# Kernel optimization log

Measured on AMD Instinct MI355X. Metric: run time of the kernel, lower is better.

Reference implementation:

```python
import jax, jax.numpy as jnp
import numpy as np
from jax import lax

NL, C, NH, LV, NPT, DFF = 6, 256, 8, 4, 4, 1024
DH = C // NH
SHAPES = np.array([[100, 100], [50, 50], [25, 25], [13, 13]], dtype=np.int32)
STARTS = np.concatenate([[0], np.cumsum(SHAPES[:, 0] * SHAPES[:, 1])[:-1]]).astype(np.int32)
S_TOT = int((SHAPES[:, 0] * SHAPES[:, 1]).sum())
TOPK = 30


def _ln(x, g, b, eps=1e-5):
    m = x.mean(-1, keepdims=True)
    v = ((x - m) ** 2).mean(-1, keepdims=True)
    return (x - m) * lax.rsqrt(v + eps) * g + b


def _mha(q, k, v, Wqkv, bqkv, Wo, bo):
    # torch nn.MultiheadAttention math (batch-first view), dropout=eval
    N, Q, _ = q.shape
    def proj(x, W, b):
        return (x @ W.T + b).reshape(N, -1, NH, DH)
    qh = proj(q, Wqkv[:C], bqkv[:C]) * (DH ** -0.5)
    kh = proj(k, Wqkv[C:2 * C], bqkv[C:2 * C])
    vh = proj(v, Wqkv[2 * C:], bqkv[2 * C:])
    a = jax.nn.softmax(jnp.einsum('bqhd,bkhd->bhqk', qh, kh), axis=-1)
    o = jnp.einsum('bhqk,bkhd->bqhd', a, vh).reshape(N, Q, C)
    return o @ Wo + bo


def _bilinear(img, gx, gy):
    # img [B,H,W,D]; gx,gy [B,P] pixel coords; grid_sample align_corners=False, zero pad
    B, Hh, Ww, D = img.shape
    x0 = jnp.floor(gx)
    y0 = jnp.floor(gy)
    wx = gx - x0
    wy = gy - y0
    bidx = jnp.arange(B)[:, None]
    def tap(xi, yi):
        inb = (xi >= 0) & (xi < Ww) & (yi >= 0) & (yi < Hh)
        v = img[bidx, jnp.clip(yi, 0, Hh - 1).astype(jnp.int32), jnp.clip(xi, 0, Ww - 1).astype(jnp.int32)]
        return v * inb[..., None]
    return (tap(x0, y0) * ((1 - wx) * (1 - wy))[..., None]
            + tap(x0 + 1, y0) * (wx * (1 - wy))[..., None]
            + tap(x0, y0 + 1) * ((1 - wx) * wy)[..., None]
            + tap(x0 + 1, y0 + 1) * (wx * wy)[..., None])


def _msda(q, ref, src, Wv, bv, Woff, boff, Waw, baw, Wo, bo):
    # MSDeformAttn: value proj, per-query sampling offsets + softmax weights,
    # multi-level bilinear sampling, weighted sum, output proj.
    N, Q, _ = q.shape
    value = (src @ Wv + bv).reshape(N, S_TOT, NH, DH)
    off = (q @ Woff + boff).reshape(N, Q, NH, LV, NPT, 2)
    aw = jax.nn.softmax((q @ Waw + baw).reshape(N, Q, NH, LV * NPT), -1).reshape(N, Q, NH, LV, NPT)
    norm = jnp.asarray(SHAPES[:, ::-1], jnp.float32)  # (W_l, H_l)
    loc = ref[:, :, None, :, None, :] + off / norm[None, None, None, :, None, :]
    acc = jnp.zeros((N * NH, Q, DH), src.dtype)
    for l in range(LV):
        H_, W_ = int(SHAPES[l, 0]), int(SHAPES[l, 1])
        s = int(STARTS[l])
        v_l = value[:, s:s + H_ * W_].transpose(0, 2, 1, 3).reshape(N * NH, H_, W_, DH)
        gx = loc[:, :, :, l, :, 0].transpose(0, 2, 1, 3).reshape(N * NH, Q * NPT) * W_ - 0.5
        gy = loc[:, :, :, l, :, 1].transpose(0, 2, 1, 3).reshape(N * NH, Q * NPT) * H_ - 0.5
        samp = _bilinear(v_l, gx, gy).reshape(N * NH, Q, NPT, DH)
        w_l = aw[:, :, :, l].transpose(0, 2, 1, 3).reshape(N * NH, Q, NPT)
        acc = acc + (samp * w_l[..., None]).sum(2)
    out = acc.reshape(N, NH, Q, DH).transpose(0, 2, 1, 3).reshape(N, Q, C)
    return out @ Wo + bo, loc, aw


def _decoder(tgt, reference_points, src, valid_ratios, query_pos, P):
    ref_in = reference_points[:, :, None] * valid_ratios[:, None]  # [N,Q,LV,2]
    out = tgt
    for i in range(NL):
        q = out + query_pos
        sa = _mha(q, q, out, P['Wqkv'][i], P['bqkv'][i], P['Wmo'][i], P['bmo'][i])
        out = _ln(out + sa, P['ln2g'][i], P['ln2b'][i])
        ca, loc, aw = _msda(out + query_pos, ref_in, src, P['Wv'][i], P['bv'][i], P['Woff'][i],
                            P['boff'][i], P['Waw'][i], P['baw'][i], P['Wo'][i], P['bo'][i])
        out = _ln(out + ca, P['ln1g'][i], P['ln1b'][i])
        ffn = jax.nn.relu(out @ P['W1'][i] + P['b1'][i]) @ P['W2'][i] + P['b2'][i]
        out = _ln(out + ffn, P['ln3g'][i], P['ln3b'][i])
        loc = loc / valid_ratios[:, None, None, :, None, :]
    N, Q = loc.shape[:2]
    wflat = aw.reshape(N, Q, -1)           # [N,Q,NH*LV*NPT]
    sflat = loc.reshape(N, Q, -1, 2)
    _, top_idx = lax.top_k(wflat, TOPK)
    samples_keep = jnp.take_along_axis(sflat, top_idx[..., None], axis=2)
    return out, reference_points, samples_keep


def setup_inputs() -> dict:
    key = jax.random.key(0)
    ks = iter(jax.random.split(key, 64))
    N, Q = 4, 300
    d = {}
    d['tgt'] = jax.random.normal(next(ks), (N, Q, C), jnp.float32)
    d['reference_points'] = jax.random.uniform(next(ks), (N, Q, 2), jnp.float32)
    d['src'] = jax.random.normal(next(ks), (N, S_TOT, C), jnp.float32)
    d['src_spatial_shapes'] = jnp.asarray(SHAPES, jnp.int32)
    d['src_level_start_index'] = jnp.asarray(STARTS, jnp.int32)
    d['src_valid_ratios'] = jnp.ones((N, LV, 2), jnp.float32)
    d['query_pos'] = jax.random.normal(next(ks), (N, Q, C), jnp.float32) * 0.02
    def p(shape, scale=0.02):
        return jax.random.normal(next(ks), shape, jnp.float32) * scale
    d['Wv'] = p((NL, C, C)); d['bv'] = jnp.zeros((NL, C))
    d['Woff'] = p((NL, C, NH * LV * NPT * 2)); d['boff'] = p((NL, NH * LV * NPT * 2), 0.1)
    d['Waw'] = p((NL, C, NH * LV * NPT)); d['baw'] = jnp.zeros((NL, NH * LV * NPT))
    d['Wo'] = p((NL, C, C)); d['bo'] = jnp.zeros((NL, C))
    d['Wqkv'] = p((NL, 3 * C, C)); d['bqkv'] = jnp.zeros((NL, 3 * C))
    d['Wmo'] = p((NL, C, C)); d['bmo'] = jnp.zeros((NL, C))
    for n in ('ln1', 'ln2', 'ln3'):
        d[n + 'g'] = jnp.ones((NL, C)); d[n + 'b'] = jnp.zeros((NL, C))
    d['W1'] = p((NL, C, DFF)); d['b1'] = jnp.zeros((NL, DFF))
    d['W2'] = p((NL, DFF, C)); d['b2'] = jnp.zeros((NL, C))
    return d


def reference(tgt, reference_points, src, src_spatial_shapes, src_level_start_index,
              src_valid_ratios, query_pos, Wv, bv, Woff, boff, Waw, baw, Wo, bo,
              Wqkv, bqkv, Wmo, bmo, ln1g, ln1b, ln2g, ln2b, ln3g, ln3b, W1, b1, W2, b2):
    # src_spatial_shapes / src_level_start_index are static (SHAPES/STARTS)
    P = dict(Wv=Wv, bv=bv, Woff=Woff, boff=boff, Waw=Waw, baw=baw, Wo=Wo, bo=bo,
             Wqkv=Wqkv, bqkv=bqkv, Wmo=Wmo, bmo=bmo, ln1g=ln1g, ln1b=ln1b,
             ln2g=ln2g, ln2b=ln2b, ln3g=ln3g, ln3b=ln3b, W1=W1, b1=b1, W2=W2, b2=b2)
    return _decoder(tgt, reference_points, src, src_valid_ratios, query_pos, P)
```

## Files before the change

### kernel.cpp

```cpp
#include <hip/hip_runtime.h>
#include <hip/hip_bf16.h>
#include <math.h>

constexpr int kNL = 6, kC = 256, kNH = 8, kDH = 32, kLV = 4, kNPT = 4;
constexpr int kDFF = 1024, kNB = 4, kNQ = 300, kSTOT = 13294, kTOPK = 30;
constexpr int kNTOK = kNB * kNQ;
constexpr int kMV = kNB * kSTOT;

constexpr size_t kWST      = 950272;
constexpr size_t OFF_QKV   = 0;
constexpr size_t OFF_MO    = 196608;
constexpr size_t OFF_OFFAW = 262144;
constexpr size_t OFF_O     = 360448;
constexpr size_t OFF_W1    = 425984;
constexpr size_t OFF_W2    = 688128;

constexpr size_t A_KH = 0;
constexpr size_t A_KL = 311296;
constexpr size_t A_VH = 622592;
constexpr size_t A_VL = 950272;
constexpr size_t A_TOT = 1277952;

typedef __bf16 bf16x8 __attribute__((ext_vector_type(8)));
typedef float f32x4 __attribute__((ext_vector_type(4)));

__device__ __forceinline__ unsigned short f2bf(float f) {
  unsigned int u = __float_as_uint(f);
  unsigned int r = (u + 0x7fffu + ((u >> 16) & 1u)) >> 16;
  return (unsigned short)r;
}
__device__ __forceinline__ void split2(float x, unsigned short& h, unsigned short& l) {
  h = f2bf(x);
  float hf = __uint_as_float(((unsigned int)h) << 16);
  l = f2bf(x - hf);
}
union BF8 { unsigned short u[8]; bf16x8 v; };

constexpr int SB_PREP = 1200;
constexpr int SB_CSRC = 13294;
constexpr int SB_CWV  = 1536;
constexpr int SB_WQ   = 4608;
constexpr int SB_T1   = 384;
constexpr int SB_T2   = 384;
constexpr int SB_T3   = 192;
constexpr int SB_T4   = 384;
constexpr int SB_T5   = 1536;
constexpr int SB_T6   = 1536;
constexpr int SB_VPAD = 80;
constexpr int SB_TOTAL = SB_PREP + SB_CSRC + SB_CWV + SB_WQ + SB_T1 + SB_T2 +
                         SB_T3 + SB_T4 + SB_T5 + SB_T6 + SB_VPAD;

__device__ __forceinline__ void wsplitT_body(
    const float* __restrict__ src, unsigned short* __restrict__ dh,
    unsigned short* __restrict__ dl, int K, int N, size_t dstOff,
    int idx, int nbx, int nby, float t[32][33], int tid) {
  const int bx = idx % nbx;
  const int by = (idx / nbx) % nby;
  const int layer = idx / (nbx * nby);
  const int nb = bx * 32, kb = by * 32;
  const float* s = src + (size_t)layer * K * N;
  unsigned short* ph = dh + (size_t)layer * kWST + dstOff;
  unsigned short* pl = dl + (size_t)layer * kWST + dstOff;
  const int tx = tid & 31, ty = tid >> 5;
  for (int i = ty; i < 32; i += 8)
    t[i][tx] = s[(size_t)(kb + i) * N + nb + tx];
  __syncthreads();
  for (int i = ty; i < 32; i += 8) {
    unsigned short h, l;
    split2(t[tx][i], h, l);
    ph[(size_t)(nb + i) * K + kb + tx] = h;
    pl[(size_t)(nb + i) * K + kb + tx] = l;
  }
}

__global__ __launch_bounds__(256) void setup_kernel(
    const float* __restrict__ tgt, const float* __restrict__ qpos,
    float* __restrict__ out_buf, float* __restrict__ qbuf,
    const float* __restrict__ src, unsigned short* __restrict__ src_bf,
    const float* __restrict__ Wv, unsigned short* __restrict__ wv_bf,
    const float* __restrict__ Wqkv, const float* __restrict__ Wmo,
    const float* __restrict__ Woff, const float* __restrict__ Waw,
    const float* __restrict__ Wo, const float* __restrict__ W1,
    const float* __restrict__ W2,
    unsigned short* __restrict__ whi, unsigned short* __restrict__ wlo,
    unsigned short* __restrict__ KV) {
  __shared__ float t[32][33];
  const int tid = threadIdx.x;
  int b = blockIdx.x;

  if (b < SB_PREP) {
    int i = b * 256 + tid;
    float v = tgt[i];
    out_buf[i] = v;
    qbuf[i] = v + qpos[i];
    return;
  }
  b -= SB_PREP;
  if (b < SB_CSRC) {
    int i = b * 256 + tid;
    float4 v = ((const float4*)src)[i];
    ushort4 o;
    o.x = f2bf(v.x); o.y = f2bf(v.y); o.z = f2bf(v.z); o.w = f2bf(v.w);
    ((ushort4*)src_bf)[i] = o;
    return;
  }
  b -= SB_CSRC;
  if (b < SB_CWV) {
    int l = b >> 8, n = b & 255, k = tid;
    wv_bf[(size_t)b * 256 + k] = f2bf(Wv[((size_t)l * 256 + k) * 256 + n]);
    return;
  }
  b -= SB_CWV;
  if (b < SB_WQ) {
    int layer = b / 768;
    int i = (b % 768) * 256 + tid;
    float v = Wqkv[(size_t)layer * 196608 + i];
    unsigned short h, l;
    split2(v, h, l);
    whi[(size_t)layer * kWST + OFF_QKV + i] = h;
    wlo[(size_t)layer * kWST + OFF_QKV + i] = l;
    return;
  }
  b -= SB_WQ;
  if (b < SB_T1) { wsplitT_body(Wmo,  whi, wlo, 256, 256,  OFF_MO,    b, 8,  8, t, tid); return; }
  b -= SB_T1;
  if (b < SB_T2) { wsplitT_body(Woff, whi, wlo, 256, 256,  OFF_OFFAW, b, 8,  8, t, tid); return; }
  b -= SB_T2;
  if (b < SB_T3) { wsplitT_body(Waw,  whi, wlo, 256, 128,  OFF_OFFAW + 256 * 256, b, 4, 8, t, tid); return; }
  b -= SB_T3;
  if (b < SB_T4) { wsplitT_body(Wo,   whi, wlo, 256, 256,  OFF_O,     b, 8,  8, t, tid); return; }
  b -= SB_T4;
  if (b < SB_T5) { wsplitT_body(W1,   whi, wlo, 256, 1024, OFF_W1,    b, 32, 8, t, tid); return; }
  b -= SB_T5;
  if (b < SB_T6) { wsplitT_body(W2,   whi, wlo, 1024, 256, OFF_W2,    b, 8, 32, t, tid); return; }
  b -= SB_T6;
  {
    int i = b * 256 + tid;
    if (i < 32 * 32 * 20) {
      int j = 300 + i % 20;
      int rest = i / 20;
      size_t idx = (size_t)rest * 320 + j;
      KV[A_VH + idx] = 0;
      KV[A_VL + idx] = 0;
    }
  }
}

template <bool RELU, int CM>
__global__ __launch_bounds__(256) void gemm_pw(
    const float* __restrict__ A,
    const unsigned short* __restrict__ BH, const unsigned short* __restrict__ BL,
    const float* __restrict__ bias, float* __restrict__ C1,
    float* __restrict__ C2,
    int M, int N, int K) {
  constexpr int LDK = 40;
  __shared__ __align__(16) unsigned short Ah[2][64 * LDK], Al[2][64 * LDK];
  __shared__ __align__(16) unsigned short Bh[2][64 * LDK], Bl[2][64 * LDK];
  const int tid = threadIdx.x;
  const int wid = tid >> 6, lane = tid & 63;
  const int wm = wid & 1, wn = wid >> 1;
  const int quad = lane >> 4, l16 = lane & 15;
  const int m0 = blockIdx.y * 64, n0 = blockIdx.x * 64;
  f32x4 acc[2][2] = {};

  const int r = tid >> 2, seg = tid & 3;
  int gr = m0 + r;
  if (gr >= M) gr = M - 1;
  const float* aRow = A + (size_t)gr * K + seg * 8;
  const unsigned short* bhRow = BH + (size_t)(n0 + r) * K + seg * 8;
  const unsigned short* blRow = BL + (size_t)(n0 + r) * K + seg * 8;

  float4 ra0 = *(const float4*)(aRow);
  float4 ra1 = *(const float4*)(aRow + 4);
  uint4 rbh = *(const uint4*)(bhRow);
  uint4 rbl = *(const uint4*)(blRow);

  {
    float xs[8] = {ra0.x, ra0.y, ra0.z, ra0.w, ra1.x, ra1.y, ra1.z, ra1.w};
    unsigned short h[8], l[8];
#pragma unroll
    for (int i = 0; i < 8; ++i) split2(xs[i], h[i], l[i]);
    *(ushort4*)&Ah[0][r * LDK + seg * 8] = make_ushort4(h[0], h[1], h[2], h[3]);
    *(ushort4*)&Ah[0][r * LDK + seg * 8 + 4] = make_ushort4(h[4], h[5], h[6], h[7]);
    *(ushort4*)&Al[0][r * LDK + seg * 8] = make_ushort4(l[0], l[1], l[2], l[3]);
    *(ushort4*)&Al[0][r * LDK + seg * 8 + 4] = make_ushort4(l[4], l[5], l[6], l[7]);
    *(uint4*)&Bh[0][r * LDK + seg * 8] = rbh;
    *(uint4*)&Bl[0][r * LDK + seg * 8] = rbl;
  }
  if (K > 32) {
    ra0 = *(const float4*)(aRow + 32);
    ra1 = *(const float4*)(aRow + 36);
    rbh = *(const uint4*)(bhRow + 32);
    rbl = *(const uint4*)(blRow + 32);
  }
  __syncthreads();

  const int NK = K / 32;
  for (int ks = 0; ks < NK; ++ks) {
    const int cur = ks & 1;
    if (ks + 1 < NK) {
      float xs[8] = {ra0.x, ra0.y, ra0.z, ra0.w, ra1.x, ra1.y, ra1.z, ra1.w};
      unsigned short h[8], l[8];
#pragma unroll
      for (int i = 0; i < 8; ++i) split2(xs[i], h[i], l[i]);
      *(ushort4*)&Ah[cur ^ 1][r * LDK + seg * 8] = make_ushort4(h[0], h[1], h[2], h[3]);
      *(ushort4*)&Ah[cur ^ 1][r * LDK + seg * 8 + 4] = make_ushort4(h[4], h[5], h[6], h[7]);
      *(ushort4*)&Al[cur ^ 1][r * LDK + seg * 8] = make_ushort4(l[0], l[1], l[2], l[3]);
      *(ushort4*)&Al[cur ^ 1][r * LDK + seg * 8 + 4] = make_ushort4(l[4], l[5], l[6], l[7]);
      *(uint4*)&Bh[cur ^ 1][r * LDK + seg * 8] = rbh;
      *(uint4*)&Bl[cur ^ 1][r * LDK + seg * 8] = rbl;
      if (ks + 2 < NK) {
        ra0 = *(const float4*)(aRow + (ks + 2) * 32);
        ra1 = *(const float4*)(aRow + (ks + 2) * 32 + 4);
        rbh = *(const uint4*)(bhRow + (ks + 2) * 32);
        rbl = *(const uint4*)(blRow + (ks + 2) * 32);
      }
    }
    bf16x8 ah[2], al[2], bh[2], bl[2];
#pragma unroll
    for (int mt = 0; mt < 2; ++mt) {
      ah[mt] = *(const bf16x8*)&Ah[cur][(wm * 32 + mt * 16 + l16) * LDK + quad * 8];
      al[mt] = *(const bf16x8*)&Al[cur][(wm * 32 + mt * 16 + l16) * LDK + quad * 8];
    }
#pragma unroll
    for (int nt = 0; nt < 2; ++nt) {
      bh[nt] = *(const bf16x8*)&Bh[cur][(wn * 32 + nt * 16 + l16) * LDK + quad * 8];
      bl[nt] = *(const bf16x8*)&Bl[cur][(wn * 32 + nt * 16 + l16) * LDK + quad * 8];
    }
#pragma unroll
    for (int mt = 0; mt < 2; ++mt)
#pragma unroll
      for (int nt = 0; nt < 2; ++nt) {
        acc[mt][nt] = __builtin_amdgcn_mfma_f32_16x16x32_bf16(ah[mt], bh[nt], acc[mt][nt], 0, 0, 0);
        acc[mt][nt] = __builtin_amdgcn_mfma_f32_16x16x32_bf16(ah[mt], bl[nt], acc[mt][nt], 0, 0, 0);
        acc[mt][nt] = __builtin_amdgcn_mfma_f32_16x16x32_bf16(al[mt], bh[nt], acc[mt][nt], 0, 0, 0);
      }
    __syncthreads();
  }

  float bc[2];
#pragma unroll
  for (int nt = 0; nt < 2; ++nt) {
    int col = n0 + wn * 32 + nt * 16 + l16;
    bc[nt] = (CM == 3 && col >= 256) ? 0.f : bias[col];
  }
#pragma unroll
  for (int mt = 0; mt < 2; ++mt) {
#pragma unroll
    for (int i = 0; i < 4; ++i) {
      int row = m0 + wm * 32 + mt * 16 + quad * 4 + i;
      if (row < M) {
#pragma unroll
        for (int nt = 0; nt < 2; ++nt) {
          int col = n0 + wn * 32 + nt * 16 + l16;
          float val = acc[mt][nt][i] + bc[nt];
          if (RELU) val = fmaxf(val, 0.f);
          if (CM == 3) {
            if (col < 256) C1[(size_t)row * 256 + col] = val;
            else C2[(size_t)row * 128 + col - 256] = val;
          } else {
            C1[(size_t)row * N + col] = val;
          }
        }
      }
    }
  }
}

__global__ __launch_bounds__(256) void qkv_value_kernel(
    const float* __restrict__ A, const float* __restrict__ A2,
    const unsigned short* __restrict__ BH, const unsigned short* __restrict__ BL,
    const float* __restrict__ bias, float* __restrict__ C1,
    unsigned short* __restrict__ C3,
    const unsigned short* __restrict__ Abf, const unsigned short* __restrict__ Btbf,
    const float* __restrict__ biasv, float* __restrict__ Cv) {
  __shared__ union __align__(16) {
    struct { unsigned short Ah[2][64 * 40], Al[2][64 * 40],
                            Bh[2][64 * 40], Bl[2][64 * 40]; } q;
    struct { unsigned short As[2][128 * 32], Bs[2][128 * 32]; } v;
  } sm;
  const int tid = threadIdx.x;
  const int wid = tid >> 6, lane = tid & 63;
  const int quad = lane >> 4, l16 = lane & 15;

  if (blockIdx.x < 228) {
    constexpr int LDK = 40, M = 1200, K = 256;
    const int m0 = (blockIdx.x / 12) * 64, n0 = (blockIdx.x % 12) * 64;
    const int wm = wid & 1, wn = wid >> 1;
    const float* Ause = (n0 >= 512) ? A2 : A;
    f32x4 acc[2][2] = {};

    const int r = tid >> 2, seg = tid & 3;
    int gr = m0 + r;
    if (gr >= M) gr = M - 1;
    const float* aRow = Ause + (size_t)gr * K + seg * 8;
    const unsigned short* bhRow = BH + (size_t)(n0 + r) * K + seg * 8;
    const unsigned short* blRow = BL + (size_t)(n0 + r) * K + seg * 8;

    float4 ra0 = *(const float4*)(aRow);
    float4 ra1 = *(const float4*)(aRow + 4);
    uint4 rbh = *(const uint4*)(bhRow);
    uint4 rbl = *(const uint4*)(blRow);
    {
      float xs[8] = {ra0.x, ra0.y, ra0.z, ra0.w, ra1.x, ra1.y, ra1.z, ra1.w};
      unsigned short h[8], l[8];
#pragma unroll
      for (int i = 0; i < 8; ++i) split2(xs[i], h[i], l[i]);
      *(ushort4*)&sm.q.Ah[0][r * LDK + seg * 8] = make_ushort4(h[0], h[1], h[2], h[3]);
      *(ushort4*)&sm.q.Ah[0][r * LDK + seg * 8 + 4] = make_ushort4(h[4], h[5], h[6], h[7]);
      *(ushort4*)&sm.q.Al[0][r * LDK + seg * 8] = make_ushort4(l[0], l[1], l[2], l[3]);
      *(ushort4*)&sm.q.Al[0][r * LDK + seg * 8 + 4] = make_ushort4(l[4], l[5], l[6], l[7]);
      *(uint4*)&sm.q.Bh[0][r * LDK + seg * 8] = rbh;
      *(uint4*)&sm.q.Bl[0][r * LDK + seg * 8] = rbl;
    }
    ra0 = *(const float4*)(aRow + 32);
    ra1 = *(const float4*)(aRow + 36);
    rbh = *(const uint4*)(bhRow + 32);
    rbl = *(const uint4*)(blRow + 32);
    __syncthreads();

    const int NK = K / 32;
    for (int ks = 0; ks < NK; ++ks) {
      const int cur = ks & 1;
      if (ks + 1 < NK) {
        float xs[8] = {ra0.x, ra0.y, ra0.z, ra0.w, ra1.x, ra1.y, ra1.z, ra1.w};
        unsigned short h[8], l[8];
#pragma unroll
        for (int i = 0; i < 8; ++i) split2(xs[i], h[i], l[i]);
        *(ushort4*)&sm.q.Ah[cur ^ 1][r * LDK + seg * 8] = make_ushort4(h[0], h[1], h[2], h[3]);
        *(ushort4*)&sm.q.Ah[cur ^ 1][r * LDK + seg * 8 + 4] = make_ushort4(h[4], h[5], h[6], h[7]);
        *(ushort4*)&sm.q.Al[cur ^ 1][r * LDK + seg * 8] = make_ushort4(l[0], l[1], l[2], l[3]);
        *(ushort4*)&sm.q.Al[cur ^ 1][r * LDK + seg * 8 + 4] = make_ushort4(l[4], l[5], l[6], l[7]);
        *(uint4*)&sm.q.Bh[cur ^ 1][r * LDK + seg * 8] = rbh;
        *(uint4*)&sm.q.Bl[cur ^ 1][r * LDK + seg * 8] = rbl;
        if (ks + 2 < NK) {
          ra0 = *(const float4*)(aRow + (ks + 2) * 32);
          ra1 = *(const float4*)(aRow + (ks + 2) * 32 + 4);
          rbh = *(const uint4*)(bhRow + (ks + 2) * 32);
          rbl = *(const uint4*)(blRow + (ks + 2) * 32);
        }
      }
      bf16x8 ah[2], al[2], bh[2], bl[2];
#pragma unroll
      for (int mt = 0; mt < 2; ++mt) {
        ah[mt] = *(const bf16x8*)&sm.q.Ah[cur][(wm * 32 + mt * 16 + l16) * LDK + quad * 8];
        al[mt] = *(const bf16x8*)&sm.q.Al[cur][(wm * 32 + mt * 16 + l16) * LDK + quad * 8];
      }
#pragma unroll
// ... 151 lines not shown
  for (int i = 0; i < 8; ++i) split2(qs[i], qh.u[i], ql.u[i]);

  f32x4 S[19];
#pragma unroll
  for (int t = 0; t < 19; ++t) {
    bf16x8 kh = *(const bf16x8*)&kh_g[(t * 16 + l16) * 32 + quad * 8];
    bf16x8 kl = *(const bf16x8*)&kl_g[(t * 16 + l16) * 32 + quad * 8];
    f32x4 z = {0.f, 0.f, 0.f, 0.f};
    z = __builtin_amdgcn_mfma_f32_16x16x32_bf16(qh.v, kh, z, 0, 0, 0);
    z = __builtin_amdgcn_mfma_f32_16x16x32_bf16(qh.v, kl, z, 0, 0, 0);
    z = __builtin_amdgcn_mfma_f32_16x16x32_bf16(ql.v, kh, z, 0, 0, 0);
    S[t] = z;
  }
  float mx[4] = {-1e30f, -1e30f, -1e30f, -1e30f};
#pragma unroll
  for (int t = 0; t < 19; ++t) {
#pragma unroll
    for (int i = 0; i < 4; ++i) {
      float s = S[t][i] * scale;
      if (t == 18 && l16 >= 12) s = -1e30f;
      S[t][i] = s;
      mx[i] = fmaxf(mx[i], s);
    }
  }
#pragma unroll
  for (int i = 0; i < 4; ++i) {
#pragma unroll
    for (int off = 8; off > 0; off >>= 1) mx[i] = fmaxf(mx[i], __shfl_xor(mx[i], off));
  }
  float sm[4] = {0.f, 0.f, 0.f, 0.f};
#pragma unroll
  for (int t = 0; t < 19; ++t) {
#pragma unroll
    for (int i = 0; i < 4; ++i) {
      float e = expf(S[t][i] - mx[i]);
      S[t][i] = e;
      sm[i] += e;
    }
  }
#pragma unroll
  for (int i = 0; i < 4; ++i) {
#pragma unroll
    for (int off = 8; off > 0; off >>= 1) sm[i] += __shfl_xor(sm[i], off);
  }
  f32x4 O0 = {0.f, 0.f, 0.f, 0.f}, O1 = {0.f, 0.f, 0.f, 0.f};
#pragma unroll
  for (int kt = 0; kt < 10; ++kt) {
    const int ta = 2 * kt, tb = 2 * kt + 1;
#pragma unroll
    for (int i = 0; i < 4; ++i) {
      int m = quad * 4 + i;
      unsigned short hA, lA, hB = 0, lB = 0;
      split2(S[ta][i], hA, lA);
      if (tb < 19) split2(S[tb][i], hB, lB);
      Ph[m * 40 + l16] = hA;
      Ph[m * 40 + 16 + l16] = hB;
      Pl[m * 40 + l16] = lA;
      Pl[m * 40 + 16 + l16] = lB;
    }
    bf16x8 pa = *(const bf16x8*)&Ph[l16 * 40 + quad * 8];
    bf16x8 pb2 = *(const bf16x8*)&Pl[l16 * 40 + quad * 8];
    bf16x8 vh0 = *(const bf16x8*)&vh_g[l16 * 320 + kt * 32 + quad * 8];
    bf16x8 vl0 = *(const bf16x8*)&vl_g[l16 * 320 + kt * 32 + quad * 8];
    bf16x8 vh1 = *(const bf16x8*)&vh_g[(16 + l16) * 320 + kt * 32 + quad * 8];
    bf16x8 vl1 = *(const bf16x8*)&vl_g[(16 + l16) * 320 + kt * 32 + quad * 8];
    O0 = __builtin_amdgcn_mfma_f32_16x16x32_bf16(pa, vh0, O0, 0, 0, 0);
    O0 = __builtin_amdgcn_mfma_f32_16x16x32_bf16(pa, vl0, O0, 0, 0, 0);
    O0 = __builtin_amdgcn_mfma_f32_16x16x32_bf16(pb2, vh0, O0, 0, 0, 0);
    O1 = __builtin_amdgcn_mfma_f32_16x16x32_bf16(pa, vh1, O1, 0, 0, 0);
    O1 = __builtin_amdgcn_mfma_f32_16x16x32_bf16(pa, vl1, O1, 0, 0, 0);
    O1 = __builtin_amdgcn_mfma_f32_16x16x32_bf16(pb2, vh1, O1, 0, 0, 0);
  }
#pragma unroll
  for (int i = 0; i < 4; ++i) {
    int q = q0 + quad * 4 + i;
    if (q < kNQ) {
      float inv = 1.f / sm[i];
      o[(size_t)(n * kNQ + q) * 256 + h * 32 + l16] = O0[i] * inv;
      o[(size_t)(n * kNQ + q) * 256 + h * 32 + 16 + l16] = O1[i] * inv;
    }
  }
}

__global__ __launch_bounds__(256) void add_ln_kernel(
    const float* __restrict__ x, const float* __restrict__ r,
    const float* __restrict__ g, const float* __restrict__ b,
    float* __restrict__ y, const float* __restrict__ qp, float* __restrict__ yq) {
  const int row = blockIdx.x * 4 + (threadIdx.x >> 6);
  const int lane = threadIdx.x & 63;
  if (row >= kNTOK) return;
  float4 xv = ((const float4*)(x + (size_t)row * kC))[lane];
  float4 rv = ((const float4*)(r + (size_t)row * kC))[lane];
  float4 v;
  v.x = xv.x + rv.x; v.y = xv.y + rv.y; v.z = xv.z + rv.z; v.w = xv.w + rv.w;
  float sum = v.x + v.y + v.z + v.w;
#pragma unroll
  for (int off = 32; off > 0; off >>= 1) sum += __shfl_xor(sum, off);
  float mean = sum * (1.f / 256.f);
  float dx = v.x - mean, dy = v.y - mean, dz = v.z - mean, dw = v.w - mean;
  float ss = dx * dx + dy * dy + dz * dz + dw * dw;
#pragma unroll
  for (int off = 32; off > 0; off >>= 1) ss += __shfl_xor(ss, off);
  float rs = rsqrtf(ss * (1.f / 256.f) + 1e-5f);
  float4 gv = ((const float4*)g)[lane];
  float4 bv = ((const float4*)b)[lane];
  float4 o;
  o.x = dx * rs * gv.x + bv.x;
  o.y = dy * rs * gv.y + bv.y;
  o.z = dz * rs * gv.z + bv.z;
  o.w = dw * rs * gv.w + bv.w;
  ((float4*)(y + (size_t)row * kC))[lane] = o;
  if (qp != nullptr) {
    float4 qv = ((const float4*)(qp + (size_t)row * kC))[lane];
    float4 t;
    t.x = o.x + qv.x; t.y = o.y + qv.y; t.z = o.z + qv.z; t.w = o.w + qv.w;
    ((float4*)(yq + (size_t)row * kC))[lane] = t;
  }
}

__global__ __launch_bounds__(256) void msda_kernel(
    const float* __restrict__ offraw, const float* __restrict__ awraw,
    const float* __restrict__ value, const float* __restrict__ refp,
    const float* __restrict__ vr, float* __restrict__ ca) {
  const int wid = threadIdx.x >> 6;
  const int lane = threadIdx.x & 63;
  const int gw = blockIdx.x * 4 + wid;
  const int h = gw % kNH;
  const int q = (gw / kNH) % kNQ;
  const int n = gw / (kNH * kNQ);
  const int half = lane >> 5, d = lane & 31;

  const float* ab = awraw + (size_t)(n * kNQ + q) * 128 + h * 16;
  float m = -1e30f;
#pragma unroll
  for (int i = 0; i < 16; ++i) m = fmaxf(m, ab[i]);
  float s = 0.f;
#pragma unroll
  for (int i = 0; i < 16; ++i) s += expf(ab[i] - m);
  const float inv = 1.f / s;

  const float rx = refp[(n * kNQ + q) * 2];
  const float ry = refp[(n * kNQ + q) * 2 + 1];
  const float* ob = offraw + (size_t)(n * kNQ + q) * 256 + h * 32;

  float acc = 0.f;
#pragma unroll
  for (int si = 0; si < 8; ++si) {
    int sp = half * 8 + si;
    int l = sp >> 2;
    float Wl = (l == 0) ? 100.f : (l == 1) ? 50.f : (l == 2) ? 25.f : 13.f;
    int Wi = (l == 0) ? 100 : (l == 1) ? 50 : (l == 2) ? 25 : 13;
    int sl = (l == 0) ? 0 : (l == 1) ? 10000 : (l == 2) ? 12500 : 13125;
    float vrx = vr[(n * kLV + l) * 2];
    float vry = vr[(n * kLV + l) * 2 + 1];
    float ox = ob[sp * 2], oy = ob[sp * 2 + 1];
    float ws = expf(ab[sp] - m) * inv;
    float gx = (rx * vrx + ox / Wl) * Wl - 0.5f;
    float gy = (ry * vry + oy / Wl) * Wl - 0.5f;
    float x0f = floorf(gx), y0f = floorf(gy);
    int x0 = (int)x0f, y0 = (int)y0f;
    float wx = gx - x0f, wy = gy - y0f;
    size_t vb = ((size_t)n * kSTOT + sl) * 256 + h * 32 + d;
#pragma unroll
    for (int t = 0; t < 4; ++t) {
      int xi = x0 + (t & 1), yi = y0 + (t >> 1);
      float wt = ((t & 1) ? wx : 1.f - wx) * ((t >> 1) ? wy : 1.f - wy);
      if (xi >= 0 && xi < Wi && yi >= 0 && yi < Wi)
        acc += ws * wt * value[vb + (size_t)(yi * Wi + xi) * 256];
    }
  }
  acc += __shfl_down(acc, 32);
  if (half == 0) ca[(size_t)(n * kNQ + q) * 256 + h * 32 + d] = acc;
}

constexpr int TB_FIN = 1210;

__global__ __launch_bounds__(256) void tail_kernel(
    const float* __restrict__ out_buf, const float* __restrict__ refp,
    const float* __restrict__ awraw, const float* __restrict__ offraw,
    const float* __restrict__ vr, float* __restrict__ dout) {
  if (blockIdx.x < TB_FIN) {
    int i = blockIdx.x * 256 + threadIdx.x;
    if (i < kNTOK * kC) dout[i] = out_buf[i];
    else if (i < kNTOK * kC + kNB * kNQ * 2) dout[i] = refp[i - kNTOK * kC];
    return;
  }
  float* outs = dout + kNTOK * kC + kNB * kNQ * 2;
  const int wid = threadIdx.x >> 6;
  const int lane = threadIdx.x & 63;
  const int gw = (blockIdx.x - TB_FIN) * 4 + wid;
  const int n = gw / kNQ, q = gw % kNQ;
  const float* ab = awraw + (size_t)(n * kNQ + q) * 128;
  float wv[2];
#pragma unroll
  for (int t = 0; t < 2; ++t) {
    int j = lane + t * 64;
    const float* hb = ab + (j >> 4) * 16;
    float m = -1e30f;
#pragma unroll
    for (int i = 0; i < 16; ++i) m = fmaxf(m, hb[i]);
    float s = 0.f, mine = 0.f;
#pragma unroll
    for (int i = 0; i < 16; ++i) {
      float e = expf(hb[i] - m);
      s += e;
      if (i == (j & 15)) mine = e;
    }
    wv[t] = mine / s;
  }
  const float rx = refp[(n * kNQ + q) * 2];
  const float ry = refp[(n * kNQ + q) * 2 + 1];
  const float* ob = offraw + (size_t)(n * kNQ + q) * 256;
  for (int k = 0; k < kTOPK; ++k) {
    float bvv;
    int bi;
    if (wv[1] > wv[0]) { bvv = wv[1]; bi = lane + 64; }
    else { bvv = wv[0]; bi = lane; }
#pragma unroll
    for (int off = 32; off > 0; off >>= 1) {
      float ov = __shfl_xor(bvv, off);
      int oi = __shfl_xor(bi, off);
      if (ov > bvv || (ov == bvv && oi < bi)) { bvv = ov; bi = oi; }
    }
    if ((bi & 63) == lane) {
      if (bi >= 64) wv[1] = -1e30f; else wv[0] = -1e30f;
    }
    if (lane == 0) {
      int l = (bi >> 2) & 3;
      float Wl = (l == 0) ? 100.f : (l == 1) ? 50.f : (l == 2) ? 25.f : 13.f;
      float vrx = vr[(n * kLV + l) * 2];
      float vry = vr[(n * kLV + l) * 2 + 1];
      float ox = ob[bi * 2], oy = ob[bi * 2 + 1];
      float lx = (rx * vrx + ox / Wl) / vrx;
      float ly = (ry * vry + oy / Wl) / vry;
      size_t base = ((size_t)(n * kNQ + q) * kTOPK + k) * 2;
      outs[base] = lx;
      outs[base + 1] = ly;
    }
  }
}

static inline dim3 sgrid(int M, int N) { return dim3((N + 63) / 64, (M + 63) / 64); }

extern "C" void kernel_launch(void* const* d_in, const int* in_sizes, int n_in,
                              void* d_out, int out_size, void* d_ws, size_t ws_size,
                              hipStream_t stream) {
  const float* tgt  = (const float*)d_in[0];
  const float* refp = (const float*)d_in[1];
  const float* src  = (const float*)d_in[2];
  const float* vr   = (const float*)d_in[5];
  const float* qpos = (const float*)d_in[6];
  const float* Wv   = (const float*)d_in[7];
  const float* bv   = (const float*)d_in[8];
  const float* Woff = (const float*)d_in[9];
  const float* boff = (const float*)d_in[10];
  const float* Waw  = (const float*)d_in[11];
  const float* Wo   = (const float*)d_in[13];
  const float* bo   = (const float*)d_in[14];
  const float* Wqkv = (const float*)d_in[15];
  const float* bqkv = (const float*)d_in[16];
  const float* Wmo  = (const float*)d_in[17];
  const float* bmo  = (const float*)d_in[18];
  const float* ln1g = (const float*)d_in[19];
  const float* ln1b = (const float*)d_in[20];
  const float* ln2g = (const float*)d_in[21];
  const float* ln2b = (const float*)d_in[22];
  const float* ln3g = (const float*)d_in[23];
  const float* ln3b = (const float*)d_in[24];
  const float* W1   = (const float*)d_in[25];
  const float* b1   = (const float*)d_in[26];
  const float* W2   = (const float*)d_in[27];
  const float* b2   = (const float*)d_in[28];
  float* out = (float*)d_out;

  float* p = (float*)d_ws;
  float* out_buf = p; p += (size_t)kNTOK * kC;
  float* qbuf    = p; p += (size_t)kNTOK * kC;
  float* qatt    = p; p += (size_t)kNTOK * kC;
  float* attn_o  = p; p += (size_t)kNTOK * kC;
  float* proj    = p; p += (size_t)kNTOK * kC;
  float* offraw  = p; p += (size_t)kNTOK * kC;
  float* awraw   = p; p += (size_t)kNTOK * 128;
  float* ca_in   = p; p += (size_t)kNTOK * kC;
  float* ffn_h   = p; p += (size_t)kNTOK * kDFF;
  float* value   = p; p += (size_t)kMV * kC;
  unsigned short* src_bf = (unsigned short*)p;
  unsigned short* wv_bf  = src_bf + (size_t)kMV * kC;
  unsigned short* whi    = wv_bf + (size_t)kNL * kC * kC;
  unsigned short* wlo    = whi + (size_t)kNL * kWST;
  unsigned short* KV     = wlo + (size_t)kNL * kWST;

  setup_kernel<<<SB_TOTAL, 256, 0, stream>>>(
      tgt, qpos, out_buf, qbuf, src, src_bf, Wv, wv_bf,
      Wqkv, Wmo, Woff, Waw, Wo, W1, W2, whi, wlo, KV);

  for (int i = 0; i < kNL; ++i) {
    const unsigned short* WH = whi + (size_t)i * kWST;
    const unsigned short* WL = wlo + (size_t)i * kWST;
    const float* bqkv_i = bqkv + (size_t)i * 3 * kC;
    const float* bmo_i  = bmo  + (size_t)i * kC;
    const float* bv_i   = bv   + (size_t)i * kC;
    const float* boff_i = boff + (size_t)i * kC;
    const float* bo_i   = bo   + (size_t)i * kC;
    const float* b1_i   = b1   + (size_t)i * kDFF;
    const float* b2_i   = b2   + (size_t)i * kC;

    qkv_value_kernel<<<228 + 832, 256, 0, stream>>>(
        qbuf, out_buf, WH + OFF_QKV, WL + OFF_QKV, bqkv_i, qatt, KV,
        src_bf, wv_bf + (size_t)i * kC * kC, bv_i, value);
    attn_kernel<<<32 * 19, 64, 0, stream>>>(qatt, KV, attn_o);
    gemm_pw<false, 0><<<sgrid(kNTOK, kC), 256, 0, stream>>>(
        attn_o, WH + OFF_MO, WL + OFF_MO, bmo_i, proj, nullptr,
        kNTOK, kC, kC);
    add_ln_kernel<<<kNTOK / 4, 256, 0, stream>>>(proj, out_buf, ln2g + (size_t)i * kC,
                                                 ln2b + (size_t)i * kC, out_buf, qpos, qbuf);
    gemm_pw<false, 3><<<sgrid(kNTOK, 384), 256, 0, stream>>>(
        qbuf, WH + OFF_OFFAW, WL + OFF_OFFAW, boff_i, offraw, awraw,
        kNTOK, 384, kC);
    msda_kernel<<<(kNB * kNQ * kNH) / 4, 256, 0, stream>>>(
        offraw, awraw, value, refp, vr, ca_in);
    gemm_pw<false, 0><<<sgrid(kNTOK, kC), 256, 0, stream>>>(
        ca_in, WH + OFF_O, WL + OFF_O, bo_i, proj, nullptr,
        kNTOK, kC, kC);
    add_ln_kernel<<<kNTOK / 4, 256, 0, stream>>>(proj, out_buf, ln1g + (size_t)i * kC,
                                                 ln1b + (size_t)i * kC, out_buf, nullptr, nullptr);
    gemm_pw<true, 0><<<sgrid(kNTOK, kDFF), 256, 0, stream>>>(
        out_buf, WH + OFF_W1, WL + OFF_W1, b1_i, ffn_h, nullptr,
        kNTOK, kDFF, kC);
    gemm_pw<false, 0><<<sgrid(kNTOK, kC), 256, 0, stream>>>(
        ffn_h, WH + OFF_W2, WL + OFF_W2, b2_i, proj, nullptr,
        kNTOK, kC, kDFF);
    add_ln_kernel<<<kNTOK / 4, 256, 0, stream>>>(proj, out_buf, ln3g + (size_t)i * kC,
                                                 ln3b + (size_t)i * kC, out_buf, qpos, qbuf);
  }

  tail_kernel<<<TB_FIN + kNB * kNQ / 4, 256, 0, stream>>>(
      out_buf, refp, awraw, offraw, vr, out);
}
```

Measured before the change: 984.8 us.

## Fuse per-layer GEMM and add-LayerNorm launches using inter-block atomic counters

Replaces the separate gemm_pw and add_ln launches in each decoder layer with two fused kernels. Inside them, blocks assigned to different stages wait on per-row-tile atomic counters (spin-wait plus release fences), so a downstream stage can start on a tile as soon as its producer tiles finish. The aim is to remove kernel launch gaps and the idle tail between dependent small kernels. The cost is spin-wait overhead, and correctness relies on producer blocks being scheduled before consumers. A bounded spin loop could silently break out and produce wrong results if they are not.

```diff
diff --git a/kernel.cpp b/kernel.cpp
--- a/kernel.cpp
+++ b/kernel.cpp
@@ -35,6 +35,25 @@
   l = f2bf(x - hf);
 }
 union BF8 { unsigned short u[8]; bf16x8 v; };
+
+__device__ __forceinline__ void release_cnt(int* c) {
+  __syncthreads();
+  if (threadIdx.x == 0) {
+    __threadfence();
+    atomicAdd(c, 1);
+  }
+}
+__device__ __forceinline__ void spin_cnt(int* c, int tgt) {
+  if (threadIdx.x == 0) {
+    int iters = 0;
+    while (atomicAdd(c, 0) < tgt) {
+      __builtin_amdgcn_s_sleep(16);
+      if (++iters > (1 << 20)) break;
+    }
+    __threadfence();
+  }
+  __syncthreads();
+}
 
 constexpr int SB_PREP = 1200;
 constexpr int SB_CSRC = 13294;
@@ -47,8 +66,12 @@
 constexpr int SB_T5   = 1536;
 constexpr int SB_T6   = 1536;
 constexpr int SB_VPAD = 80;
+constexpr int SB_CNT  = 1;
 constexpr int SB_TOTAL = SB_PREP + SB_CSRC + SB_CWV + SB_WQ + SB_T1 + SB_T2 +
-                         SB_T3 + SB_T4 + SB_T5 + SB_T6 + SB_VPAD;
+                         SB_T3 + SB_T4 + SB_T5 + SB_T6 + SB_VPAD + SB_CNT;
+
+constexpr int kCntPerLayer = 192;
+constexpr int kCntTotal = kNL * kCntPerLayer;
 
 __device__ __forceinline__ void wsplitT_body(
     const float* __restrict__ src, unsigned short* __restrict__ dh,
@@ -83,7 +106,7 @@
     const float* __restrict__ Wo, const float* __restrict__ W1,
     const float* __restrict__ W2,
     unsigned short* __restrict__ whi, unsigned short* __restrict__ wlo,
-    unsigned short* __restrict__ KV) {
+    unsigned short* __restrict__ KV, int* __restrict__ cnt) {
   __shared__ float t[32][33];
   const int tid = threadIdx.x;
   int b = blockIdx.x;
@@ -134,7 +157,7 @@
   b -= SB_T5;
   if (b < SB_T6) { wsplitT_body(W2,   whi, wlo, 1024, 256, OFF_W2,    b, 8, 32, t, tid); return; }
   b -= SB_T6;
-  {
+  if (b < SB_VPAD) {
     int i = b * 256 + tid;
     if (i < 32 * 32 * 20) {
       int j = 300 + i % 20;
@@ -143,24 +166,31 @@
       KV[A_VH + idx] = 0;
       KV[A_VL + idx] = 0;
     }
-  }
-}
-
-template <bool RELU, int CM>
-__global__ __launch_bounds__(256) void gemm_pw(
+    return;
+  }
+#pragma unroll
+  for (int k = 0; k < 5; ++k) {
+    int i = tid + k * 256;
+    if (i < kCntTotal) cnt[i] = 0;
+  }
+}
+
+__device__ __forceinline__ void gemm_core(
     const float* __restrict__ A,
     const unsigned short* __restrict__ BH, const unsigned short* __restrict__ BL,
-    const float* __restrict__ bias, float* __restrict__ C1,
-    float* __restrict__ C2,
-    int M, int N, int K) {
+    const float* __restrict__ bias, float* __restrict__ C1, float* __restrict__ C2,
+    int M, int N, int K, int bx, int by, bool relu, bool dual,
+    unsigned short* __restrict__ lds, int* relCnt) {
   constexpr int LDK = 40;
-  __shared__ __align__(16) unsigned short Ah[2][64 * LDK], Al[2][64 * LDK];
-  __shared__ __align__(16) unsigned short Bh[2][64 * LDK], Bl[2][64 * LDK];
+  unsigned short* Ah = lds;
+  unsigned short* Al = lds + 2 * 64 * LDK;
+  unsigned short* Bh = lds + 4 * 64 * LDK;
+  unsigned short* Bl = lds + 6 * 64 * LDK;
   const int tid = threadIdx.x;
   const int wid = tid >> 6, lane = tid & 63;
   const int wm = wid & 1, wn = wid >> 1;
   const int quad = lane >> 4, l16 = lane & 15;
-  const int m0 = blockIdx.y * 64, n0 = blockIdx.x * 64;
+  const int m0 = by * 64, n0 = bx * 64;
   f32x4 acc[2][2] = {};
 
   const int r = tid >> 2, seg = tid & 3;
@@ -180,12 +210,12 @@
     unsigned short h[8], l[8];
 #pragma unroll
     for (int i = 0; i < 8; ++i) split2(xs[i], h[i], l[i]);
-    *(ushort4*)&Ah[0][r * LDK + seg * 8] = make_ushort4(h[0], h[1], h[2], h[3]);
-    *(ushort4*)&Ah[0][r * LDK + seg * 8 + 4] = make_ushort4(h[4], h[5], h[6], h[7]);
-    *(ushort4*)&Al[0][r * LDK + seg * 8] = make_ushort4(l[0], l[1], l[2], l[3]);
-    *(ushort4*)&Al[0][r * LDK + seg * 8 + 4] = make_ushort4(l[4], l[5], l[6], l[7]);
-    *(uint4*)&Bh[0][r * LDK + seg * 8] = rbh;
-    *(uint4*)&Bl[0][r * LDK + seg * 8] = rbl;
+    *(ushort4*)&Ah[r * LDK + seg * 8] = make_ushort4(h[0], h[1], h[2], h[3]);
+    *(ushort4*)&Ah[r * LDK + seg * 8 + 4] = make_ushort4(h[4], h[5], h[6], h[7]);
+    *(ushort4*)&Al[r * LDK + seg * 8] = make_ushort4(l[0], l[1], l[2], l[3]);
+    *(ushort4*)&Al[r * LDK + seg * 8 + 4] = make_ushort4(l[4], l[5], l[6], l[7]);
+    *(uint4*)&Bh[r * LDK + seg * 8] = rbh;
+    *(uint4*)&Bl[r * LDK + seg * 8] = rbl;
   }
   if (K > 32) {
     ra0 = *(const float4*)(aRow + 32);
@@ -198,17 +228,19 @@
   const int NK = K / 32;
   for (int ks = 0; ks < NK; ++ks) {
     const int cur = ks & 1;
+    const int nxt = (cur ^ 1) * 64 * LDK;
+    const int curo = cur * 64 * LDK;
     if (ks + 1 < NK) {
       float xs[8] = {ra0.x, ra0.y, ra0.z, ra0.w, ra1.x, ra1.y, ra1.z, ra1.w};
       unsigned short h[8], l[8];
 #pragma unroll
       for (int i = 0; i < 8; ++i) split2(xs[i], h[i], l[i]);
-      *(ushort4*)&Ah[cur ^ 1][r * LDK + seg * 8] = make_ushort4(h[0], h[1], h[2], h[3]);
-      *(ushort4*)&Ah[cur ^ 1][r * LDK + seg * 8 + 4] = make_ushort4(h[4], h[5], h[6], h[7]);
-      *(ushort4*)&Al[cur ^ 1][r * LDK + seg * 8] = make_ushort4(l[0], l[1], l[2], l[3]);
-      *(ushort4*)&Al[cur ^ 1][r * LDK + seg * 8 + 4] = make_ushort4(l[4], l[5], l[6], l[7]);
-      *(uint4*)&Bh[cur ^ 1][r * LDK + seg * 8] = rbh;
-      *(uint4*)&Bl[cur ^ 1][r * LDK + seg * 8] = rbl;
+      *(ushort4*)&Ah[nxt + r * LDK + seg * 8] = make_ushort4(h[0], h[1], h[2], h[3]);
+      *(ushort4*)&Ah[nxt + r * LDK + seg * 8 + 4] = make_ushort4(h[4], h[5], h[6], h[7]);
+      *(ushort4*)&Al[nxt + r * LDK + seg * 8] = make_ushort4(l[0], l[1], l[2], l[3]);
+      *(ushort4*)&Al[nxt + r * LDK + seg * 8 + 4] = make_ushort4(l[4], l[5], l[6], l[7]);
+      *(uint4*)&Bh[nxt + r * LDK + seg * 8] = rbh;
+      *(uint4*)&Bl[nxt + r * LDK + seg * 8] = rbl;
       if (ks + 2 < NK) {
         ra0 = *(const float4*)(aRow + (ks + 2) * 32);
         ra1 = *(const float4*)(aRow + (ks + 2) * 32 + 4);
@@ -219,13 +251,13 @@
     bf16x8 ah[2], al[2], bh[2], bl[2];
 #pragma unroll
     for (int mt = 0; mt < 2; ++mt) {
-      ah[mt] = *(const bf16x8*)&Ah[cur][(wm * 32 + mt * 16 + l16) * LDK + quad * 8];
-      al[mt] = *(const bf16x8*)&Al[cur][(wm * 32 + mt * 16 + l16) * LDK + quad * 8];
+      ah[mt] = *(const bf16x8*)&Ah[curo + (wm * 32 + mt * 16 + l16) * LDK + quad * 8];
+      al[mt] = *(const bf16x8*)&Al[curo + (wm * 32 + mt * 16 + l16) * LDK + quad * 8];
     }
 #pragma unroll
     for (int nt = 0; nt < 2; ++nt) {
-      bh[nt] = *(const bf16x8*)&Bh[cur][(wn * 32 + nt * 16 + l16) * LDK + quad * 8];
-      bl[nt] = *(const bf16x8*)&Bl[cur][(wn * 32 + nt * 16 + l16) * LDK + quad * 8];
+      bh[nt] = *(const bf16x8*)&Bh[curo + (wn * 32 + nt * 16 + l16) * LDK + quad * 8];
+      bl[nt] = *(const bf16x8*)&Bl[curo + (wn * 32 + nt * 16 + l16) * LDK + quad * 8];
     }
 #pragma unroll
     for (int mt = 0; mt < 2; ++mt)
@@ -242,7 +274,7 @@
 #pragma unroll
   for (int nt = 0; nt < 2; ++nt) {
     int col = n0 + wn * 32 + nt * 16 + l16;
-    bc[nt] = (CM == 3 && col >= 256) ? 0.f : bias[col];
+    bc[nt] = (dual && col >= 256) ? 0.f : bias[col];
   }
 #pragma unroll
   for (int mt = 0; mt < 2; ++mt) {
@@ -254,8 +286,8 @@
         for (int nt = 0; nt < 2; ++nt) {
           int col = n0 + wn * 32 + nt * 16 + l16;
           float val = acc[mt][nt][i] + bc[nt];
-          if (RELU) val = fmaxf(val, 0.f);
-          if (CM == 3) {
+          if (relu) val = fmaxf(val, 0.f);
+          if (dual) {
             if (col < 256) C1[(size_t)row * 256 + col] = val;
             else C2[(size_t)row * 128 + col - 256] = val;
           } else {
@@ -264,6 +296,41 @@
         }
       }
     }
+  }
+  if (relCnt) release_cnt(relCnt);
+}
+
+__device__ __forceinline__ void add_ln_core(
+    int row, const float* __restrict__ x, const float* __restrict__ r,
+    const float* __restrict__ g, const float* __restrict__ b,
+    float* __restrict__ y, const float* __restrict__ qp, float* __restrict__ yq,
+    int lane) {
+  float4 xv = ((const float4*)(x + (size_t)row * kC))[lane];
+  float4 rv = ((const float4*)(r + (size_t)row * kC))[lane];
+  float4 v;
+  v.x = xv.x + rv.x; v.y = xv.y + rv.y; v.z = xv.z + rv.z; v.w = xv.w + rv.w;
+  float sum = v.x + v.y + v.z + v.w;
+#pragma unroll
+  for (int off = 32; off > 0; off >>= 1) sum += __shfl_xor(sum, off);
+  float mean = sum * (1.f / 256.f);
+  float dx = v.x - mean, dy = v.y - mean, dz = v.z - mean, dw = v.w - mean;
+  float ss = dx * dx + dy * dy + dz * dz + dw * dw;
+#pragma unroll
+  for (int off = 32; off > 0; off >>= 1) ss += __shfl_xor(ss, off);
+  float rs = rsqrtf(ss * (1.f / 256.f) + 1e-5f);
+  float4 gv = ((const float4*)g)[lane];
+  float4 bv = ((const float4*)b)[lane];
+  float4 o;
+  o.x = dx * rs * gv.x + bv.x;
+  o.y = dy * rs * gv.y + bv.y;
+  o.z = dz * rs * gv.z + bv.z;
+  o.w = dw * rs * gv.w + bv.w;
+  ((float4*)(y + (size_t)row * kC))[lane] = o;
+  if (qp != nullptr) {
+    float4 qv = ((const float4*)(qp + (size_t)row * kC))[lane];
+    float4 t;
+    t.x = o.x + qv.x; t.y = o.y + qv.y; t.z = o.z + qv.z; t.w = o.w + qv.w;
+    ((float4*)(yq + (size_t)row * kC))[lane] = t;
   }
 }
 
@@ -581,39 +648,82 @@
   }
 }
 
-__global__ __launch_bounds__(256) void add_ln_kernel(
-    const float* __restrict__ x, const float* __restrict__ r,
-    const float* __restrict__ g, const float* __restrict__ b,
-    float* __restrict__ y, const float* __restrict__ qp, float* __restrict__ yq) {
-  const int row = blockIdx.x * 4 + (threadIdx.x >> 6);
-  const int lane = threadIdx.x & 63;
-  if (row >= kNTOK) return;
-  float4 xv = ((const float4*)(x + (size_t)row * kC))[lane];
-  float4 rv = ((const float4*)(r + (size_t)row * kC))[lane];
-  float4 v;
-  v.x = xv.x + rv.x; v.y = xv.y + rv.y; v.z = xv.z + rv.z; v.w = xv.w + rv.w;
-  float sum = v.x + v.y + v.z + v.w;
-#pragma unroll
-  for (int off = 32; off > 0; off >>= 1) sum += __shfl_xor(sum, off);
-  float mean = sum * (1.f / 256.f);
-  float dx = v.x - mean, dy = v.y - mean, dz = v.z - mean, dw = v.w - mean;
-  float ss = dx * dx + dy * dy + dz * dz + dw * dw;
-#pragma unroll
-  for (int off = 32; off > 0; off >>= 1) ss += __shfl_xor(ss, off);
-  float rs = rsqrtf(ss * (1.f / 256.f) + 1e-5f);
-  float4 gv = ((const float4*)g)[lane];
-  float4 bv = ((const float4*)b)[lane];
-  float4 o;
-  o.x = dx * rs * gv.x + bv.x;
-  o.y = dy * rs * gv.y + bv.y;
-  o.z = dz * rs * gv.z + bv.z;
-  o.w = dw * rs * gv.w + bv.w;
-  ((float4*)(y + (size_t)row * kC))[lane] = o;
-  if (qp != nullptr) {
-    float4 qv = ((const float4*)(qp + (size_t)row * kC))[lane];
-    float4 t;
-    t.x = o.x + qv.x; t.y = o.y + qv.y; t.z = o.z + qv.z; t.w = o.w + qv.w;
-    ((float4*)(yq + (size_t)row * kC))[lane] = t;
+__global__ __launch_bounds__(256) void fuseA_kernel(
+    const float* __restrict__ attn_o,
+    const unsigned short* __restrict__ WH, const unsigned short* __restrict__ WL,
+    const float* __restrict__ bmo, float* __restrict__ proj,
+    float* __restrict__ out_buf, const float* __restrict__ ln2g,
+    const float* __restrict__ ln2b, const float* __restrict__ qpos,
+    float* __restrict__ qbuf, const float* __restrict__ boff,
+    float* __restrict__ offraw, float* __restrict__ awraw,
+    int* __restrict__ cnt) {
+  __shared__ __align__(16) unsigned short lds[8 * 64 * 40];
+  const int b = blockIdx.x;
+  if (b < 76) {
+    gemm_core(attn_o, WH + OFF_MO, WL + OFF_MO, bmo, proj, nullptr,
+              kNTOK, 256, 256, b & 3, b >> 2, false, false, lds, &cnt[0 + (b >> 2)]);
+  } else if (b < 151) {
+    const int j = b - 76, tile = j >> 2;
+    spin_cnt(&cnt[0 + tile], 4);
+    const int wid = threadIdx.x >> 6, lane = threadIdx.x & 63;
+#pragma unroll
+    for (int rr = 0; rr < 4; ++rr)
+      add_ln_core(j * 16 + wid * 4 + rr, proj, out_buf, ln2g, ln2b,
+                  out_buf, qpos, qbuf, lane);
+    release_cnt(&cnt[32 + tile]);
+  } else {
+    const int idx = b - 151;
+    const int bx = idx % 6, by = idx / 6;
+    spin_cnt(&cnt[32 + by], (by == 18) ? 3 : 4);
+    gemm_core(qbuf, WH + OFF_OFFAW, WL + OFF_OFFAW, boff, offraw, awraw,
+              kNTOK, 384, 256, bx, by, false, true, lds, nullptr);
+  }
+}
+
+__global__ __launch_bounds__(256) void fuseB_kernel(
+    const float* __restrict__ ca_in,
+    const unsigned short* __restrict__ WH, const unsigned short* __restrict__ WL,
+    const float* __restrict__ bo, float* __restrict__ proj,
+    float* __restrict__ out_buf, const float* __restrict__ ln1g,
+    const float* __restrict__ ln1b, const float* __restrict__ b1,
+    float* __restrict__ ffn_h, const float* __restrict__ b2,
+    const float* __restrict__ ln3g, const float* __restrict__ ln3b,
+    const float* __restrict__ qpos, float* __restrict__ qbuf,
+    int* __restrict__ cnt) {
+  __shared__ __align__(16) unsigned short lds[8 * 64 * 40];
+  const int b = blockIdx.x;
+  if (b < 76) {
+    gemm_core(ca_in, WH + OFF_O, WL + OFF_O, bo, proj, nullptr,
+              kNTOK, 256, 256, b & 3, b >> 2, false, false, lds, &cnt[64 + (b >> 2)]);
+  } else if (b < 151) {
+    const int j = b - 76, tile = j >> 2;
+    spin_cnt(&cnt[64 + tile], 4);
+    const int wid = threadIdx.x >> 6, lane = threadIdx.x & 63;
+#pragma unroll
+    for (int rr = 0; rr < 4; ++rr)
+      add_ln_core(j * 16 + wid * 4 + rr, proj, out_buf, ln1g, ln1b,
+                  out_buf, nullptr, nullptr, lane);
+    release_cnt(&cnt[96 + tile]);
+  } else if (b < 455) {
+    const int idx = b - 151;
+    const int bx = idx & 15, by = idx >> 4;
+    spin_cnt(&cnt[96 + by], (by == 18) ? 3 : 4);
+    gemm_core(out_buf, WH + OFF_W1, WL + OFF_W1, b1, ffn_h, nullptr,
+              kNTOK, 1024, 256, bx, by, true, false, lds, &cnt[128 + by]);
+  } else if (b < 531) {
+    const int idx = b - 455;
+    const int bx = idx & 3, by = idx >> 2;
+    spin_cnt(&cnt[128 + by], 16);
+    gemm_core(ffn_h, WH + OFF_W2, WL + OFF_W2, b2, proj, nullptr,
+              kNTOK, 256, 1024, bx, by, false, false, lds, &cnt[160 + by]);
+  } else {
+    const int j = b - 531, tile = j >> 2;
+    spin_cnt(&cnt[160 + tile], 4);
+    const int wid = threadIdx.x >> 6, lane = threadIdx.x & 63;
+#pragma unroll
+    for (int rr = 0; rr < 4; ++rr)
+      add_ln_core(j * 16 + wid * 4 + rr, proj, out_buf, ln3g, ln3b,
+                  out_buf, qpos, qbuf, lane);
   }
 }
 
@@ -738,8 +848,6 @@
     }
   }
 }
-
-static inline dim3 sgrid(int M, int N) { return dim3((N + 63) / 64, (M + 63) / 64); }
 
 extern "C" void kernel_launch(void* const* d_in, const int* in_sizes, int n_in,
                               void* d_out, int out_size, void* d_ws, size_t ws_size,
@@ -788,10 +896,11 @@
   unsigned short* whi    = wv_bf + (size_t)kNL * kC * kC;
   unsigned short* wlo    = whi + (size_t)kNL * kWST;
   unsigned short* KV     = wlo + (size_t)kNL * kWST;
+  int* cntbuf            = (int*)(KV + A_TOT);
 
   setup_kernel<<<SB_TOTAL, 256, 0, stream>>>(
       tgt, qpos, out_buf, qbuf, src, src_bf, Wv, wv_bf,
-      Wqkv, Wmo, Woff, Waw, Wo, W1, W2, whi, wlo, KV);
+      Wqkv, Wmo, Woff, Waw, Wo, W1, W2, whi, wlo, KV, cntbuf);
 
   for (int i = 0; i < kNL; ++i) {
     const unsigned short* WH = whi + (size_t)i * kWST;
@@ -803,34 +912,22 @@
     const float* bo_i   = bo   + (size_t)i * kC;
     const float* b1_i   = b1   + (size_t)i * kDFF;
     const float* b2_i   = b2   + (size_t)i * kC;
+    int* cnt_i = cntbuf + i * kCntPerLayer;
 
     qkv_value_kernel<<<228 + 832, 256, 0, stream>>>(
         qbuf, out_buf, WH + OFF_QKV, WL + OFF_QKV, bqkv_i, qatt, KV,
         src_bf, wv_bf + (size_t)i * kC * kC, bv_i, value);
     attn_kernel<<<32 * 19, 64, 0, stream>>>(qatt, KV, attn_o);
-    gemm_pw<false, 0><<<sgrid(kNTOK, kC), 256, 0, stream>>>(
-        attn_o, WH + OFF_MO, WL + OFF_MO, bmo_i, proj, nullptr,
-        kNTOK, kC, kC);
-    add_ln_kernel<<<kNTOK / 4, 256, 0, stream>>>(proj, out_buf, ln2g + (size_t)i * kC,
-                                                 ln2b + (size_t)i * kC, out_buf, qpos, qbuf);
-    gemm_pw<false, 3><<<sgrid(kNTOK, 384), 256, 0, stream>>>(
-        qbuf, WH + OFF_OFFAW, WL + OFF_OFFAW, boff_i, offraw, awraw,
-        kNTOK, 384, kC);
+    fuseA_kernel<<<265, 256, 0, stream>>>(
+        attn_o, WH, WL, bmo_i, proj, out_buf,
+        ln2g + (size_t)i * kC, ln2b + (size_t)i * kC, qpos, qbuf,
+        boff_i, offraw, awraw, cnt_i);
     msda_kernel<<<(kNB * kNQ * kNH) / 4, 256, 0, stream>>>(
         offraw, awraw, value, refp, vr, ca_in);
-    gemm_pw<false, 0><<<sgrid(kNTOK, kC), 256, 0, stream>>>(
-        ca_in, WH + OFF_O, WL + OFF_O, bo_i, proj, nullptr,
-        kNTOK, kC, kC);
-    add_ln_kernel<<<kNTOK / 4, 256, 0, stream>>>(proj, out_buf, ln1g + (size_t)i * kC,
-                                                 ln1b + (size_t)i * kC, out_buf, nullptr, nullptr);
-    gemm_pw<true, 0><<<sgrid(kNTOK, kDFF), 256, 0, stream>>>(
-        out_buf, WH + OFF_W1, WL + OFF_W1, b1_i, ffn_h, nullptr,
-        kNTOK, kDFF, kC);
-    gemm_pw<false, 0><<<sgrid(kNTOK, kC), 256, 0, stream>>>(
-        ffn_h, WH + OFF_W2, WL + OFF_W2, b2_i, proj, nullptr,
-        kNTOK, kC, kDFF);
-    add_ln_kernel<<<kNTOK / 4, 256, 0, stream>>>(proj, out_buf, ln3g + (size_t)i * kC,
-                                                 ln3b + (size_t)i * kC, out_buf, qpos, qbuf);
+    fuseB_kernel<<<606, 256, 0, stream>>>(
+        ca_in, WH, WL, bo_i, proj, out_buf,
+        ln1g + (size_t)i * kC, ln1b + (size_t)i * kC, b1_i, ffn_h, b2_i,
+        ln3g + (size_t)i * kC, ln3b + (size_t)i * kC, qpos, qbuf, cnt_i);
   }
 
   tail_kernel<<<TB_FIN + kNB * kNQ / 4, 256, 0, stream>>>(
```

New measurement: 1.345 ms. 36.6% more time.
